# Kernel tuning notes

Hardware: AMD Instinct MI355X
Metric: run time of the kernel (lower is better)

Reference implementation:

```python
import jax, jax.numpy as jnp
import numpy as np

B, S, H = 1, 2048, 2048
E, I = 16, 1408
I_SHARED = 5632
TOP_K = 2


def setup_inputs() -> dict:
    key = jax.random.key(0)
    ks = jax.random.split(key, 8)
    scale = 0.02
    return {
        "hidden_states": jax.random.normal(ks[0], (B, S, H), dtype=jnp.float32),
        "router_w": jax.random.normal(ks[1], (H, E), dtype=jnp.float32) * scale,
        "expert_gate_up_w": jax.random.normal(ks[2], (E, H, 2 * I), dtype=jnp.float32) * scale,
        "expert_out_w": jax.random.normal(ks[3], (E, I, H), dtype=jnp.float32) * scale,
        "shared_ffw_gate_w": jax.random.normal(ks[4], (H, I_SHARED), dtype=jnp.float32) * scale,
        "shared_ffw_inter_w": jax.random.normal(ks[5], (H, I_SHARED), dtype=jnp.float32) * scale,
        "shared_ffw_out_w": jax.random.normal(ks[6], (I_SHARED, H), dtype=jnp.float32) * scale,
        "shared_gate_w": jax.random.normal(ks[7], (H, 1), dtype=jnp.float32) * scale,
        "top_k": TOP_K,
    }


def reference(hidden_states, router_w, expert_gate_up_w, expert_out_w,
              shared_ffw_gate_w, shared_ffw_inter_w, shared_ffw_out_w,
              shared_gate_w, top_k):
    b, s, h = hidden_states.shape
    e = router_w.shape[-1]
    x = hidden_states.reshape(-1, h)  # [T, H]

    # --- Router: softmax over experts, top-k, renormalize (norm_top_k_prob=True) ---
    router_logits = x @ router_w                        # [T, E]
    router_probs = jax.nn.softmax(router_logits, -1)
    top_p, top_i = jax.lax.top_k(router_probs, top_k)   # [T, K]
    top_p = top_p / jnp.sum(top_p, axis=-1, keepdims=True)
    # dense routing matrix [E, T] (matches one_hot-sum-transpose in source)
    one_hot = jax.nn.one_hot(top_i, e, dtype=top_p.dtype)  # [T, K, E]
    routing_full = jnp.sum(one_hot * top_p[..., None], axis=1).T  # [E, T]

    # --- Dense per-expert SwiGLU over ALL tokens (as in QwenMoeExperts) ---
    gate_up = jnp.einsum('th,ehm->etm', x, expert_gate_up_w)  # [E, T, 2I]
    gate, up = jnp.split(gate_up, 2, axis=-1)
    hidden = up * jax.nn.silu(gate)                           # [E, T, I]
    expert_out = jnp.einsum('eti,eih->eth', hidden, expert_out_w)  # [E, T, H]
    expert_contribution = jnp.einsum('eth,et->th', expert_out, routing_full)

    # --- Shared expert (SwiGLU MLP) with sigmoid gate ---
    sgate = jax.nn.silu(x @ shared_ffw_gate_w)
    sinter = x @ shared_ffw_inter_w
    shared_out = (sinter * sgate) @ shared_ffw_out_w          # [T, H]
    shared_out = shared_out * jax.nn.sigmoid(x @ shared_gate_w)

    out = (expert_contribution + shared_out).reshape(b, s, h)
    return out, router_logits
```

## Files before the change

kernel.cpp:

```cpp
#include <hip/hip_runtime.h>
#include <math.h>

typedef __attribute__((ext_vector_type(4))) float f32x4;
typedef __attribute__((ext_vector_type(2))) unsigned int u32x2;
typedef __attribute__((ext_vector_type(4))) unsigned int u32x4;
typedef __attribute__((ext_vector_type(8))) unsigned short u16x8;
typedef __attribute__((ext_vector_type(8))) __bf16 bf16x8;
typedef unsigned short ushort_t;

#define H_DIM 2048
#define T_TOK 2048
#define NEXP 16
#define I_DIM 1408
#define I2_DIM 2816
#define IS_DIM 5632
#define MAXROWS 6144
#define LDT 40

static __device__ __forceinline__ unsigned short f2bf(float f){
  union { float f; unsigned u; } v; v.f = f;
  unsigned r = v.u + 0x7FFFu + ((v.u >> 16) & 1u);
  return (unsigned short)(r >> 16);
}
static __device__ __forceinline__ float bf2f(unsigned short h){
  union { unsigned u; float f; } v; v.u = ((unsigned)h) << 16;
  return v.f;
}
static __device__ __forceinline__ float silu_f(float x){ return x / (1.f + __expf(-x)); }

__global__ void cast_bf16_k(const float* __restrict__ in, ushort_t* __restrict__ out){
  long i = ((long)blockIdx.x * 256 + threadIdx.x) * 8;
  f32x4 a = *(const f32x4*)&in[i];
  f32x4 b = *(const f32x4*)&in[i + 4];
  union { ushort_t s[8]; u32x4 v; } pk;
  #pragma unroll
  for (int j = 0; j < 4; j++){ pk.s[j] = f2bf(a[j]); pk.s[j+4] = f2bf(b[j]); }
  *(u32x4*)&out[i] = pk.v;
}

__global__ void transpose_cast_k(const float* __restrict__ in, ushort_t* __restrict__ out,
                                 int K, int N){
  long zo = (long)blockIdx.z * K * N;
  in += zo; out += zo;
  __shared__ float tl[32][33];
  int n0 = blockIdx.x * 32, k0 = blockIdx.y * 32;
  int tid = threadIdx.x;
  int tx = tid & 31, ty = tid >> 5;
  #pragma unroll
  for (int j = 0; j < 4; j++)
    tl[ty + j*8][tx] = in[(long)(k0 + ty + j*8) * N + n0 + tx];
  __syncthreads();
  int nl = tid >> 3, kc = (tid & 7) * 4;
  unsigned w0 = (unsigned)f2bf(tl[kc+0][nl]) | ((unsigned)f2bf(tl[kc+1][nl]) << 16);
  unsigned w1 = (unsigned)f2bf(tl[kc+2][nl]) | ((unsigned)f2bf(tl[kc+3][nl]) << 16);
  u32x2 o; o[0] = w0; o[1] = w1;
  *(u32x2*)&out[(long)(n0 + nl) * K + k0 + kc] = o;
}

__global__ void router_k(const float* __restrict__ x, const float* __restrict__ rw,
                         const float* __restrict__ sgw, float* __restrict__ logits,
                         int* __restrict__ counts, int* __restrict__ lists,
                         float* __restrict__ probs, float* __restrict__ sgmul){
  int wid = threadIdx.x >> 6, lane = threadIdx.x & 63;
  int t = blockIdx.x * 4 + wid;
  const float* xr = x + (long)t * H_DIM;
  float acc[17];
  #pragma unroll
  for (int e = 0; e < 17; e++) acc[e] = 0.f;
  for (int h0 = lane * 4; h0 < H_DIM; h0 += 256){
    f32x4 xv = *(const f32x4*)&xr[h0];
    #pragma unroll
    for (int i = 0; i < 4; i++){
      float xs = xv[i];
      const float* wrow = rw + (long)(h0 + i) * NEXP;
      #pragma unroll
      for (int e = 0; e < 16; e++) acc[e] += xs * wrow[e];
      acc[16] += xs * sgw[h0 + i];
    }
  }
  #pragma unroll
  for (int e = 0; e < 17; e++)
    for (int off = 32; off >= 1; off >>= 1)
      acc[e] += __shfl_xor(acc[e], off);
  if (lane == 0){
    float* lo = logits + (long)t * NEXP;
    #pragma unroll
    for (int e = 0; e < 16; e++) lo[e] = acc[e];
    int e0 = 0;
    #pragma unroll
    for (int e = 1; e < 16; e++) if (acc[e] > acc[e0]) e0 = e;
    int e1 = (e0 == 0) ? 1 : 0;
    #pragma unroll
    for (int e = 0; e < 16; e++) if (e != e0 && acc[e] > acc[e1]) e1 = e;
    float d = acc[e1] - acc[e0];
    float ed = __expf(d);
    float p0 = 1.f / (1.f + ed);
    float p1 = ed / (1.f + ed);
    int pos0 = atomicAdd(&counts[e0], 1);
    lists[e0 * T_TOK + pos0] = t; probs[e0 * T_TOK + pos0] = p0;
    int pos1 = atomicAdd(&counts[e1], 1);
    lists[e1 * T_TOK + pos1] = t; probs[e1 * T_TOK + pos1] = p1;
    sgmul[t] = 1.f / (1.f + __expf(-acc[16]));
  }
}

__global__ void bases_k(const int* __restrict__ counts, int* __restrict__ bases){
  if (threadIdx.x == 0){
    int r = 0;
    for (int e = 0; e < NEXP; e++){ bases[e] = r; r += (counts[e] + 127) & ~127; }
  }
}

__global__ void swiglu_expert_k(const ushort_t* __restrict__ gu, ushort_t* __restrict__ hid){
  long q = (long)blockIdx.x * 256 + threadIdx.x;
  long r = q / (I_DIM / 8); int ic = (int)(q % (I_DIM / 8)) * 8;
  const ushort_t* g = gu + r * I2_DIM + ic;
  u16x8 gv = *(const u16x8*)g;
  u16x8 uv = *(const u16x8*)(g + I_DIM);
  u16x8 ov;
  #pragma unroll
  for (int i = 0; i < 8; i++)
    ov[i] = f2bf(bf2f(uv[i]) * silu_f(bf2f(gv[i])));
  *(u16x8*)&hid[r * I_DIM + ic] = ov;
}

__global__ void swiglu_flat_k(ushort_t* __restrict__ sg, const ushort_t* __restrict__ si){
  long i = ((long)blockIdx.x * 256 + threadIdx.x) * 8;
  u16x8 g = *(const u16x8*)&sg[i];
  u16x8 s = *(const u16x8*)&si[i];
  u16x8 o;
  #pragma unroll
  for (int j = 0; j < 8; j++)
    o[j] = f2bf(bf2f(s[j]) * silu_f(bf2f(g[j])));
  *(u16x8*)&sg[i] = o;
}

template<int MODE>
__global__ void gemm_k(const ushort_t* __restrict__ A, const ushort_t* __restrict__ Bt,
                       ushort_t* __restrict__ Cb,
                       int M, int N, int K, int lda, int ldbt, int ldc,
                       const int* __restrict__ counts, const int* __restrict__ bases,
                       const int* __restrict__ lists, const float* __restrict__ probs,
                       const float* __restrict__ svec, float* __restrict__ outp,
                       long bstride){
  int z = blockIdx.z;
  int cnt = M;
  const ushort_t* Ab = A;
  const ushort_t* Bb = Bt;
  long rbase = 0;
  if constexpr (MODE == 1){ cnt = counts[z]; rbase = bases[z]; Bb += (long)z * bstride; }
  if constexpr (MODE == 2){ cnt = counts[z]; Ab += (long)bases[z] * lda; Bb += (long)z * bstride; }
  int m0 = blockIdx.y * 128;
  if (m0 >= cnt) return;
  int n0 = blockIdx.x * 128;

  __shared__ ushort_t As[128 * LDT];
  __shared__ ushort_t Bs[128 * LDT];

  int tid = threadIdx.x;
  int lane = tid & 63;
  int wr = (tid >> 7) & 1;
  int wc = (tid >> 6) & 1;

  int srow[2], skc[2];
  long aoff[2], boff[2];
  #pragma unroll
  for (int p = 0; p < 2; p++){
    int idx = p * 256 + tid;
    srow[p] = idx >> 2;
    skc[p]  = (idx & 3) * 8;
    int j = m0 + srow[p];
    if constexpr (MODE == 1){
      int jj = j < cnt ? j : cnt - 1;
      aoff[p] = (long)lists[z * T_TOK + jj] * lda + skc[p];
    } else {
      aoff[p] = (long)j * lda + skc[p];
    }
    boff[p] = (long)(n0 + srow[p]) * ldbt + skc[p];
  }

  u32x4 ar[2], br[2];
  #pragma unroll
  for (int p = 0; p < 2; p++){
    ar[p] = *(const u32x4*)(Ab + aoff[p]);
    br[p] = *(const u32x4*)(Bb + boff[p]);
  }

  f32x4 zero = {0.f, 0.f, 0.f, 0.f};
  f32x4 acc[4][4];
  #pragma unroll
  for (int i = 0; i < 4; i++)
    #pragma unroll
    for (int j = 0; j < 4; j++) acc[i][j] = zero;

  int nsteps = K / 32;
  for (int s = 0; s < nsteps; s++){
    __syncthreads();
    #pragma unroll
    for (int p = 0; p < 2; p++){
      *(u32x4*)&As[srow[p] * LDT + skc[p]] = ar[p];
      *(u32x4*)&Bs[srow[p] * LDT + skc[p]] = br[p];
    }
    __syncthreads();
    if (s + 1 < nsteps){
      int k0 = (s + 1) * 32;
      #pragma unroll
      for (int p = 0; p < 2; p++){
        ar[p] = *(const u32x4*)(Ab + aoff[p] + k0);
        br[p] = *(const u32x4*)(Bb + boff[p] + k0);
      }
    }
    bf16x8 af[4], bv[4];
    #pragma unroll
    for (int f = 0; f < 4; f++){
      af[f] = *(const bf16x8*)&As[(wr * 64 + f * 16 + (lane & 15)) * LDT + (lane >> 4) * 8];
      bv[f] = *(const bf16x8*)&Bs[(wc * 64 + f * 16 + (lane & 15)) * LDT + (lane >> 4) * 8];
    }
    #pragma unroll
    for (int fm = 0; fm < 4; fm++)
      #pragma unroll
      for (int fn = 0; fn < 4; fn++)
        acc[fm][fn] = __builtin_amdgcn_mfma_f32_16x16x32_bf16(af[fm], bv[fn], acc[fm][fn], 0, 0, 0);
  }

  int colb = n0 + wc * 64 + (lane & 15);
  int rowb = m0 + wr * 64 + (lane >> 4) * 4;
  #pragma unroll
  for (int fm = 0; fm < 4; fm++){
    #pragma unroll
    for (int fn = 0; fn < 4; fn++){
      f32x4 v = acc[fm][fn];
      int col = colb + fn * 16;
      #pragma unroll
      for (int r = 0; r < 4; r++){
        int m = rowb + fm * 16 + r;
        if constexpr (MODE == 0){
          Cb[(long)m * ldc + col] = f2bf(v[r]);
        } else if constexpr (MODE == 1){
          if (m < cnt) Cb[(rbase + m) * (long)ldc + col] = f2bf(v[r]);
        } else if constexpr (MODE == 2){
          if (m < cnt){
            int tok = lists[z * T_TOK + m];
            float p = probs[z * T_TOK + m];
            atomicAdd(outp + (long)tok * ldc + col, p * v[r]);
          }
        } else {
          outp[(long)m * ldc + col] = svec[m] * v[r];
        }
      }
    }
  }
}

extern "C" void kernel_launch(void* const* d_in, const int* in_sizes, int n_in,
                              void* d_out, int out_size, void* d_ws, size_t ws_size,
                              hipStream_t stream){
  const float* x    = (const float*)d_in[0];
  const float* rw   = (const float*)d_in[1];
  const float* wgu  = (const float*)d_in[2];
  const float* wout = (const float*)d_in[3];
  const float* wsg  = (const float*)d_in[4];
  const float* wsi  = (const float*)d_in[5];
  const float* wso  = (const float*)d_in[6];
  const float* sgw  = (const float*)d_in[7];

  float* out = (float*)d_out;
  float* logits = out + (size_t)T_TOK * H_DIM;

  char* w = (char*)d_ws;
  auto alloc = [&](size_t b){ char* p = w; w += (b + 255) & ~(size_t)255; return p; };
  ushort_t* xb     = (ushort_t*)alloc((size_t)T_TOK * H_DIM * 2);
  ushort_t* wgu_t  = (ushort_t*)alloc((size_t)NEXP * I2_DIM * H_DIM * 2);
  ushort_t* wout_t = (ushort_t*)alloc((size_t)NEXP * H_DIM * I_DIM * 2);
  ushort_t* wsg_t  = (ushort_t*)alloc((size_t)IS_DIM * H_DIM * 2);
  ushort_t* wsi_t  = (ushort_t*)alloc((size_t)IS_DIM * H_DIM * 2);
  ushort_t* wso_t  = (ushort_t*)alloc((size_t)H_DIM * IS_DIM * 2);
  ushort_t* sgr    = (ushort_t*)alloc((size_t)T_TOK * IS_DIM * 2);
  ushort_t* sir    = (ushort_t*)alloc((size_t)T_TOK * IS_DIM * 2);
  ushort_t* gu     = (ushort_t*)alloc((size_t)MAXROWS * I2_DIM * 2);
  ushort_t* hid    = (ushort_t*)alloc((size_t)MAXROWS * I_DIM * 2);
  int*   counts = (int*)alloc(64);
  int*   bases  = (int*)alloc(64);
  int*   lists  = (int*)alloc((size_t)NEXP * T_TOK * 4);
  float* probs  = (float*)alloc((size_t)NEXP * T_TOK * 4);
  float* sgmul  = (float*)alloc((size_t)T_TOK * 4);

  hipMemsetAsync(counts, 0, 64, stream);

  cast_bf16_k<<<2048, 256, 0, stream>>>(x, xb);
  transpose_cast_k<<<dim3(I2_DIM/32, H_DIM/32, NEXP), 256, 0, stream>>>(wgu, wgu_t, H_DIM, I2_DIM);
  transpose_cast_k<<<dim3(H_DIM/32, I_DIM/32, NEXP), 256, 0, stream>>>(wout, wout_t, I_DIM, H_DIM);
  transpose_cast_k<<<dim3(IS_DIM/32, H_DIM/32, 1), 256, 0, stream>>>(wsg, wsg_t, H_DIM, IS_DIM);
  transpose_cast_k<<<dim3(IS_DIM/32, H_DIM/32, 1), 256, 0, stream>>>(wsi, wsi_t, H_DIM, IS_DIM);
  transpose_cast_k<<<dim3(H_DIM/32, IS_DIM/32, 1), 256, 0, stream>>>(wso, wso_t, IS_DIM, H_DIM);

  router_k<<<512, 256, 0, stream>>>(x, rw, sgw, logits, counts, lists, probs, sgmul);
  bases_k<<<1, 64, 0, stream>>>(counts, bases);

  gemm_k<0><<<dim3(IS_DIM/128, T_TOK/128, 1), 256, 0, stream>>>(
      xb, wsg_t, sgr, T_TOK, IS_DIM, H_DIM, H_DIM, H_DIM, IS_DIM,
      nullptr, nullptr, nullptr, nullptr, nullptr, nullptr, 0);
  gemm_k<0><<<dim3(IS_DIM/128, T_TOK/128, 1), 256, 0, stream>>>(
      xb, wsi_t, sir, T_TOK, IS_DIM, H_DIM, H_DIM, H_DIM, IS_DIM,
      nullptr, nullptr, nullptr, nullptr, nullptr, nullptr, 0);
  swiglu_flat_k<<<(T_TOK * (IS_DIM/8)) / 256, 256, 0, stream>>>(sgr, sir);
  gemm_k<3><<<dim3(H_DIM/128, T_TOK/128, 1), 256, 0, stream>>>(
      sgr, wso_t, nullptr, T_TOK, H_DIM, IS_DIM, IS_DIM, IS_DIM, H_DIM,
      nullptr, nullptr, nullptr, nullptr, sgmul, out, 0);

  gemm_k<1><<<dim3(I2_DIM/128, T_TOK/128, NEXP), 256, 0, stream>>>(
      xb, wgu_t, gu, T_TOK, I2_DIM, H_DIM, H_DIM, H_DIM, I2_DIM,
      counts, bases, lists, probs, nullptr, nullptr, (long)I2_DIM * H_DIM);
  swiglu_expert_k<<<(MAXROWS * (I_DIM/8)) / 256, 256, 0, stream>>>(gu, hid);
  gemm_k<2><<<dim3(H_DIM/128, T_TOK/128, NEXP), 256, 0, stream>>>(
      hid, wout_t, nullptr, T_TOK, H_DIM, I_DIM, I_DIM, I_DIM, H_DIM,
      counts, bases, lists, probs, nullptr, out, (long)H_DIM * I_DIM);

  (void)in_sizes; (void)n_in; (void)out_size; (void)ws_size;
}
```

Baseline: 807.2 us.

## Read fp32 weights directly in GEMM, dropping separate transpose-cast pre-pass

Removes the five transpose_cast kernels that converted every weight matrix to transposed bf16 before each call. The GEMM now loads fp32 weight rows straight from the original layout, converts them to bf16 in registers, and writes them transposed into a swizzled LDS tile. The K step grows from 32 to 64, the grid is flattened with an XCD-aware block remap, and launch bounds are added. This saves a large weight read-write pass, at the cost of reading fp32 weights (twice the bytes) inside the GEMM and doing the conversion there. In MODE 1 and 2 the fp32 weights are also re-read by every M block of each expert.

```diff
diff --git a/kernel.cpp b/kernel.cpp
--- a/kernel.cpp
+++ b/kernel.cpp
@@ -1,8 +1,8 @@
 #include <hip/hip_runtime.h>
 #include <math.h>
 
+typedef __attribute__((ext_vector_type(2))) float f32x2;
 typedef __attribute__((ext_vector_type(4))) float f32x4;
-typedef __attribute__((ext_vector_type(2))) unsigned int u32x2;
 typedef __attribute__((ext_vector_type(4))) unsigned int u32x4;
 typedef __attribute__((ext_vector_type(8))) unsigned short u16x8;
 typedef __attribute__((ext_vector_type(8))) __bf16 bf16x8;
@@ -15,7 +15,6 @@
 #define I2_DIM 2816
 #define IS_DIM 5632
 #define MAXROWS 6144
-#define LDT 40
 
 static __device__ __forceinline__ unsigned short f2bf(float f){
   union { float f; unsigned u; } v; v.f = f;
@@ -27,6 +26,10 @@
   return v.f;
 }
 static __device__ __forceinline__ float silu_f(float x){ return x / (1.f + __expf(-x)); }
+
+static __device__ __forceinline__ int swz(int row, int slot){
+  return row * 64 + ((slot ^ ((row >> 1) & 7)) << 3);
+}
 
 __global__ void cast_bf16_k(const float* __restrict__ in, ushort_t* __restrict__ out){
   long i = ((long)blockIdx.x * 256 + threadIdx.x) * 8;
@@ -36,25 +39,6 @@
   #pragma unroll
   for (int j = 0; j < 4; j++){ pk.s[j] = f2bf(a[j]); pk.s[j+4] = f2bf(b[j]); }
   *(u32x4*)&out[i] = pk.v;
-}
-
-__global__ void transpose_cast_k(const float* __restrict__ in, ushort_t* __restrict__ out,
-                                 int K, int N){
-  long zo = (long)blockIdx.z * K * N;
-  in += zo; out += zo;
-  __shared__ float tl[32][33];
-  int n0 = blockIdx.x * 32, k0 = blockIdx.y * 32;
-  int tid = threadIdx.x;
-  int tx = tid & 31, ty = tid >> 5;
-  #pragma unroll
-  for (int j = 0; j < 4; j++)
-    tl[ty + j*8][tx] = in[(long)(k0 + ty + j*8) * N + n0 + tx];
-  __syncthreads();
-  int nl = tid >> 3, kc = (tid & 7) * 4;
-  unsigned w0 = (unsigned)f2bf(tl[kc+0][nl]) | ((unsigned)f2bf(tl[kc+1][nl]) << 16);
-  unsigned w1 = (unsigned)f2bf(tl[kc+2][nl]) | ((unsigned)f2bf(tl[kc+3][nl]) << 16);
-  u32x2 o; o[0] = w0; o[1] = w1;
-  *(u32x2*)&out[(long)(n0 + nl) * K + k0 + kc] = o;
 }
 
 __global__ void router_k(const float* __restrict__ x, const float* __restrict__ rw,
@@ -112,8 +96,8 @@
 }
 
 __global__ void swiglu_expert_k(const ushort_t* __restrict__ gu, ushort_t* __restrict__ hid){
-  long q = (long)blockIdx.x * 256 + threadIdx.x;
-  long r = q / (I_DIM / 8); int ic = (int)(q % (I_DIM / 8)) * 8;
+  long qd = (long)blockIdx.x * 256 + threadIdx.x;
+  long r = qd / (I_DIM / 8); int ic = (int)(qd % (I_DIM / 8)) * 8;
   const ushort_t* g = gu + r * I2_DIM + ic;
   u16x8 gv = *(const u16x8*)g;
   u16x8 uv = *(const u16x8*)(g + I_DIM);
@@ -136,54 +120,69 @@
 }
 
 template<int MODE>
-__global__ void gemm_k(const ushort_t* __restrict__ A, const ushort_t* __restrict__ Bt,
-                       ushort_t* __restrict__ Cb,
-                       int M, int N, int K, int lda, int ldbt, int ldc,
-                       const int* __restrict__ counts, const int* __restrict__ bases,
-                       const int* __restrict__ lists, const float* __restrict__ probs,
-                       const float* __restrict__ svec, float* __restrict__ outp,
-                       long bstride){
+__global__ __launch_bounds__(256, 2)
+void gemm_k(const ushort_t* __restrict__ A, const float* __restrict__ Bf,
+            ushort_t* __restrict__ Cb,
+            int K, int lda, int ldb, int ldc, int mb,
+            const int* __restrict__ counts, const int* __restrict__ bases,
+            const int* __restrict__ lists, const float* __restrict__ probs,
+            const float* __restrict__ svec, float* __restrict__ outp,
+            long bstride){
   int z = blockIdx.z;
-  int cnt = M;
+  int cnt = T_TOK;
   const ushort_t* Ab = A;
-  const ushort_t* Bb = Bt;
+  const float* Bb = Bf;
   long rbase = 0;
   if constexpr (MODE == 1){ cnt = counts[z]; rbase = bases[z]; Bb += (long)z * bstride; }
   if constexpr (MODE == 2){ cnt = counts[z]; Ab += (long)bases[z] * lda; Bb += (long)z * bstride; }
-  int m0 = blockIdx.y * 128;
+
+  int nwg = gridDim.x;
+  int wgo = blockIdx.x;
+  int q = nwg >> 3, r = nwg & 7;
+  int xcd = wgo & 7, idx = wgo >> 3;
+  int wg = (xcd < r ? xcd * (q + 1) : r * (q + 1) + (xcd - r) * q) + idx;
+  int mblk = wg % mb, nblk = wg / mb;
+  int m0 = mblk * 128;
   if (m0 >= cnt) return;
-  int n0 = blockIdx.x * 128;
-
-  __shared__ ushort_t As[128 * LDT];
-  __shared__ ushort_t Bs[128 * LDT];
+  int n0 = nblk * 128;
+
+  __shared__ ushort_t As[128 * 64];
+  __shared__ ushort_t Bs[128 * 64];
 
   int tid = threadIdx.x;
   int lane = tid & 63;
-  int wr = (tid >> 7) & 1;
-  int wc = (tid >> 6) & 1;
-
-  int srow[2], skc[2];
-  long aoff[2], boff[2];
-  #pragma unroll
-  for (int p = 0; p < 2; p++){
-    int idx = p * 256 + tid;
-    srow[p] = idx >> 2;
-    skc[p]  = (idx & 3) * 8;
-    int j = m0 + srow[p];
+  int wv = tid >> 6;
+  int wr = wv >> 1, wc = wv & 1;
+
+  const ushort_t* aptr[4];
+  int am[4], aslot[4];
+  #pragma unroll
+  for (int qq = 0; qq < 4; qq++){
+    int it = tid + qq * 256;
+    int m = it >> 3, slot = it & 7;
+    am[qq] = m; aslot[qq] = slot;
+    int row;
     if constexpr (MODE == 1){
-      int jj = j < cnt ? j : cnt - 1;
-      aoff[p] = (long)lists[z * T_TOK + jj] * lda + skc[p];
+      int j = m0 + m; if (j >= cnt) j = cnt - 1;
+      row = lists[z * T_TOK + j];
     } else {
-      aoff[p] = (long)j * lda + skc[p];
-    }
-    boff[p] = (long)(n0 + srow[p]) * ldbt + skc[p];
-  }
-
-  u32x4 ar[2], br[2];
-  #pragma unroll
-  for (int p = 0; p < 2; p++){
-    ar[p] = *(const u32x4*)(Ab + aoff[p]);
-    br[p] = *(const u32x4*)(Bb + boff[p]);
+      row = m0 + m;
+    }
+    aptr[qq] = Ab + (long)row * lda + slot * 8;
+  }
+  int p = lane;
+  int sp = wv;
+  const float* bb0 = Bb + (long)(sp * 8) * ldb + n0 + 2 * p;
+  const float* bb1 = bb0 + (long)32 * ldb;
+
+  u32x4 ar[4];
+  f32x2 br0[8], br1[8];
+  #pragma unroll
+  for (int qq = 0; qq < 4; qq++) ar[qq] = *(const u32x4*)(aptr[qq]);
+  #pragma unroll
+  for (int i = 0; i < 8; i++){
+    br0[i] = *(const f32x2*)(bb0 + (long)i * ldb);
+    br1[i] = *(const f32x2*)(bb1 + (long)i * ldb);
   }
 
   f32x4 zero = {0.f, 0.f, 0.f, 0.f};
@@ -193,34 +192,53 @@
     #pragma unroll
     for (int j = 0; j < 4; j++) acc[i][j] = zero;
 
-  int nsteps = K / 32;
+  int nsteps = K >> 6;
   for (int s = 0; s < nsteps; s++){
     __syncthreads();
     #pragma unroll
-    for (int p = 0; p < 2; p++){
-      *(u32x4*)&As[srow[p] * LDT + skc[p]] = ar[p];
-      *(u32x4*)&Bs[srow[p] * LDT + skc[p]] = br[p];
+    for (int qq = 0; qq < 4; qq++)
+      *(u32x4*)&As[swz(am[qq], aslot[qq])] = ar[qq];
+    {
+      bf16x8 c0, c1, d0, d1;
+      #pragma unroll
+      for (int i = 0; i < 8; i++){
+        c0[i] = (__bf16)br0[i][0];
+        c1[i] = (__bf16)br0[i][1];
+        d0[i] = (__bf16)br1[i][0];
+        d1[i] = (__bf16)br1[i][1];
+      }
+      *(bf16x8*)&Bs[swz(2*p,     sp)]     = c0;
+      *(bf16x8*)&Bs[swz(2*p + 1, sp)]     = c1;
+      *(bf16x8*)&Bs[swz(2*p,     sp + 4)] = d0;
+      *(bf16x8*)&Bs[swz(2*p + 1, sp + 4)] = d1;
     }
     __syncthreads();
     if (s + 1 < nsteps){
-      int k0 = (s + 1) * 32;
-      #pragma unroll
-      for (int p = 0; p < 2; p++){
-        ar[p] = *(const u32x4*)(Ab + aoff[p] + k0);
-        br[p] = *(const u32x4*)(Bb + boff[p] + k0);
+      int kt = (s + 1) * 64;
+      #pragma unroll
+      for (int qq = 0; qq < 4; qq++) ar[qq] = *(const u32x4*)(aptr[qq] + kt);
+      const float* nb0 = bb0 + (long)kt * ldb;
+      const float* nb1 = bb1 + (long)kt * ldb;
+      #pragma unroll
+      for (int i = 0; i < 8; i++){
+        br0[i] = *(const f32x2*)(nb0 + (long)i * ldb);
+        br1[i] = *(const f32x2*)(nb1 + (long)i * ldb);
       }
     }
-    bf16x8 af[4], bv[4];
-    #pragma unroll
-    for (int f = 0; f < 4; f++){
-      af[f] = *(const bf16x8*)&As[(wr * 64 + f * 16 + (lane & 15)) * LDT + (lane >> 4) * 8];
-      bv[f] = *(const bf16x8*)&Bs[(wc * 64 + f * 16 + (lane & 15)) * LDT + (lane >> 4) * 8];
-    }
-    #pragma unroll
-    for (int fm = 0; fm < 4; fm++)
-      #pragma unroll
-      for (int fn = 0; fn < 4; fn++)
-        acc[fm][fn] = __builtin_amdgcn_mfma_f32_16x16x32_bf16(af[fm], bv[fn], acc[fm][fn], 0, 0, 0);
+    #pragma unroll
+    for (int kk = 0; kk < 2; kk++){
+      bf16x8 af[4], bg[4];
+      #pragma unroll
+      for (int f = 0; f < 4; f++){
+        af[f] = *(const bf16x8*)&As[swz(wr*64 + f*16 + (lane & 15), kk*4 + (lane >> 4))];
+        bg[f] = *(const bf16x8*)&Bs[swz(wc*64 + f*16 + (lane & 15), kk*4 + (lane >> 4))];
+      }
+      #pragma unroll
+      for (int fm = 0; fm < 4; fm++)
+        #pragma unroll
+        for (int fn = 0; fn < 4; fn++)
+          acc[fm][fn] = __builtin_amdgcn_mfma_f32_16x16x32_bf16(af[fm], bg[fn], acc[fm][fn], 0, 0, 0);
+    }
   }
 
   int colb = n0 + wc * 64 + (lane & 15);
@@ -232,20 +250,20 @@
       f32x4 v = acc[fm][fn];
       int col = colb + fn * 16;
       #pragma unroll
-      for (int r = 0; r < 4; r++){
-        int m = rowb + fm * 16 + r;
+      for (int rr = 0; rr < 4; rr++){
+        int m = rowb + fm * 16 + rr;
         if constexpr (MODE == 0){
-          Cb[(long)m * ldc + col] = f2bf(v[r]);
+          Cb[(long)m * ldc + col] = f2bf(v[rr]);
         } else if constexpr (MODE == 1){
-          if (m < cnt) Cb[(rbase + m) * (long)ldc + col] = f2bf(v[r]);
+          if (m < cnt) Cb[(rbase + m) * (long)ldc + col] = f2bf(v[rr]);
         } else if constexpr (MODE == 2){
           if (m < cnt){
             int tok = lists[z * T_TOK + m];
-            float p = probs[z * T_TOK + m];
-            atomicAdd(outp + (long)tok * ldc + col, p * v[r]);
+            float pp = probs[z * T_TOK + m];
+            atomicAdd(outp + (long)tok * ldc + col, pp * v[rr]);
           }
         } else {
-          outp[(long)m * ldc + col] = svec[m] * v[r];
+          outp[(long)m * ldc + col] = svec[m] * v[rr];
         }
       }
     }
@@ -269,16 +287,11 @@
 
   char* w = (char*)d_ws;
   auto alloc = [&](size_t b){ char* p = w; w += (b + 255) & ~(size_t)255; return p; };
-  ushort_t* xb     = (ushort_t*)alloc((size_t)T_TOK * H_DIM * 2);
-  ushort_t* wgu_t  = (ushort_t*)alloc((size_t)NEXP * I2_DIM * H_DIM * 2);
-  ushort_t* wout_t = (ushort_t*)alloc((size_t)NEXP * H_DIM * I_DIM * 2);
-  ushort_t* wsg_t  = (ushort_t*)alloc((size_t)IS_DIM * H_DIM * 2);
-  ushort_t* wsi_t  = (ushort_t*)alloc((size_t)IS_DIM * H_DIM * 2);
-  ushort_t* wso_t  = (ushort_t*)alloc((size_t)H_DIM * IS_DIM * 2);
-  ushort_t* sgr    = (ushort_t*)alloc((size_t)T_TOK * IS_DIM * 2);
-  ushort_t* sir    = (ushort_t*)alloc((size_t)T_TOK * IS_DIM * 2);
-  ushort_t* gu     = (ushort_t*)alloc((size_t)MAXROWS * I2_DIM * 2);
-  ushort_t* hid    = (ushort_t*)alloc((size_t)MAXROWS * I_DIM * 2);
+  ushort_t* xb  = (ushort_t*)alloc((size_t)T_TOK * H_DIM * 2);
+  ushort_t* sgr = (ushort_t*)alloc((size_t)T_TOK * IS_DIM * 2);
+  ushort_t* sir = (ushort_t*)alloc((size_t)T_TOK * IS_DIM * 2);
+  ushort_t* gu  = (ushort_t*)alloc((size_t)MAXROWS * I2_DIM * 2);
+  ushort_t* hid = (ushort_t*)alloc((size_t)MAXROWS * I_DIM * 2);
   int*   counts = (int*)alloc(64);
   int*   bases  = (int*)alloc(64);
   int*   lists  = (int*)alloc((size_t)NEXP * T_TOK * 4);
@@ -288,33 +301,27 @@
   hipMemsetAsync(counts, 0, 64, stream);
 
   cast_bf16_k<<<2048, 256, 0, stream>>>(x, xb);
-  transpose_cast_k<<<dim3(I2_DIM/32, H_DIM/32, NEXP), 256, 0, stream>>>(wgu, wgu_t, H_DIM, I2_DIM);
-  transpose_cast_k<<<dim3(H_DIM/32, I_DIM/32, NEXP), 256, 0, stream>>>(wout, wout_t, I_DIM, H_DIM);
-  transpose_cast_k<<<dim3(IS_DIM/32, H_DIM/32, 1), 256, 0, stream>>>(wsg, wsg_t, H_DIM, IS_DIM);
-  transpose_cast_k<<<dim3(IS_DIM/32, H_DIM/32, 1), 256, 0, stream>>>(wsi, wsi_t, H_DIM, IS_DIM);
-  transpose_cast_k<<<dim3(H_DIM/32, IS_DIM/32, 1), 256, 0, stream>>>(wso, wso_t, IS_DIM, H_DIM);
-
   router_k<<<512, 256, 0, stream>>>(x, rw, sgw, logits, counts, lists, probs, sgmul);
   bases_k<<<1, 64, 0, stream>>>(counts, bases);
 
-  gemm_k<0><<<dim3(IS_DIM/128, T_TOK/128, 1), 256, 0, stream>>>(
-      xb, wsg_t, sgr, T_TOK, IS_DIM, H_DIM, H_DIM, H_DIM, IS_DIM,
+  gemm_k<0><<<dim3((IS_DIM/128) * (T_TOK/128), 1, 1), 256, 0, stream>>>(
+      xb, wsg, sgr, H_DIM, H_DIM, IS_DIM, IS_DIM, T_TOK/128,
       nullptr, nullptr, nullptr, nullptr, nullptr, nullptr, 0);
-  gemm_k<0><<<dim3(IS_DIM/128, T_TOK/128, 1), 256, 0, stream>>>(
-      xb, wsi_t, sir, T_TOK, IS_DIM, H_DIM, H_DIM, H_DIM, IS_DIM,
+  gemm_k<0><<<dim3((IS_DIM/128) * (T_TOK/128), 1, 1), 256, 0, stream>>>(
+      xb, wsi, sir, H_DIM, H_DIM, IS_DIM, IS_DIM, T_TOK/128,
       nullptr, nullptr, nullptr, nullptr, nullptr, nullptr, 0);
   swiglu_flat_k<<<(T_TOK * (IS_DIM/8)) / 256, 256, 0, stream>>>(sgr, sir);
-  gemm_k<3><<<dim3(H_DIM/128, T_TOK/128, 1), 256, 0, stream>>>(
-      sgr, wso_t, nullptr, T_TOK, H_DIM, IS_DIM, IS_DIM, IS_DIM, H_DIM,
+  gemm_k<3><<<dim3((H_DIM/128) * (T_TOK/128), 1, 1), 256, 0, stream>>>(
+      sgr, wso, nullptr, IS_DIM, IS_DIM, H_DIM, H_DIM, T_TOK/128,
       nullptr, nullptr, nullptr, nullptr, sgmul, out, 0);
 
-  gemm_k<1><<<dim3(I2_DIM/128, T_TOK/128, NEXP), 256, 0, stream>>>(
-      xb, wgu_t, gu, T_TOK, I2_DIM, H_DIM, H_DIM, H_DIM, I2_DIM,
-      counts, bases, lists, probs, nullptr, nullptr, (long)I2_DIM * H_DIM);
+  gemm_k<1><<<dim3((I2_DIM/128) * (T_TOK/128), 1, NEXP), 256, 0, stream>>>(
+      xb, wgu, gu, H_DIM, H_DIM, I2_DIM, I2_DIM, T_TOK/128,
+      counts, bases, lists, probs, nullptr, nullptr, (long)H_DIM * I2_DIM);
   swiglu_expert_k<<<(MAXROWS * (I_DIM/8)) / 256, 256, 0, stream>>>(gu, hid);
-  gemm_k<2><<<dim3(H_DIM/128, T_TOK/128, NEXP), 256, 0, stream>>>(
-      hid, wout_t, nullptr, T_TOK, H_DIM, I_DIM, I_DIM, I_DIM, H_DIM,
-      counts, bases, lists, probs, nullptr, out, (long)H_DIM * I_DIM);
+  gemm_k<2><<<dim3((H_DIM/128) * (T_TOK/128), 1, NEXP), 256, 0, stream>>>(
+      hid, wout, nullptr, I_DIM, I_DIM, H_DIM, H_DIM, T_TOK/128,
+      counts, bases, lists, probs, nullptr, out, (long)I_DIM * H_DIM);
 
   (void)in_sizes; (void)n_in; (void)out_size; (void)ws_size;
 }
```

New measurement: 826.2 us. 2.4% more time.

## Use direct global-to-LDS loads, XCD-aware tile remap, split-K and batched shared GEMMs

Applied to the files above, without the earlier changes.

Replaces register-staged tile loads with global_load_lds direct-to-LDS copies using an unpadded 32-wide LDS layout, and drops the register prefetch. Remaps flat block indices so that neighbouring tiles land on the same XCD for L2 reuse. Fuses the two shared gate/inter GEMMs into one launch via grid z, and splits K in two for the shared output GEMM, which now accumulates with atomics into a pre-zeroed output. This removes the register round trip but loses load/compute overlap, and the unpadded LDS may cause bank conflicts. The split-K path also adds atomic traffic and a memset.

```diff
diff --git a/kernel.cpp b/kernel.cpp
--- a/kernel.cpp
+++ b/kernel.cpp
@@ -15,7 +15,6 @@
 #define I2_DIM 2816
 #define IS_DIM 5632
 #define MAXROWS 6144
-#define LDT 40
 
 static __device__ __forceinline__ unsigned short f2bf(float f){
   union { float f; unsigned u; } v; v.f = f;
@@ -27,6 +26,12 @@
   return v.f;
 }
 static __device__ __forceinline__ float silu_f(float x){ return x / (1.f + __expf(-x)); }
+
+static __device__ __forceinline__ void gld16(const ushort_t* g, ushort_t* l){
+  __builtin_amdgcn_global_load_lds(
+      (const __attribute__((address_space(1))) unsigned int*)g,
+      (__attribute__((address_space(3))) unsigned int*)l, 16, 0, 0);
+}
 
 __global__ void cast_bf16_k(const float* __restrict__ in, ushort_t* __restrict__ out){
   long i = ((long)blockIdx.x * 256 + threadIdx.x) * 8;
@@ -112,8 +117,8 @@
 }
 
 __global__ void swiglu_expert_k(const ushort_t* __restrict__ gu, ushort_t* __restrict__ hid){
-  long q = (long)blockIdx.x * 256 + threadIdx.x;
-  long r = q / (I_DIM / 8); int ic = (int)(q % (I_DIM / 8)) * 8;
+  long qd = (long)blockIdx.x * 256 + threadIdx.x;
+  long r = qd / (I_DIM / 8); int ic = (int)(qd % (I_DIM / 8)) * 8;
   const ushort_t* g = gu + r * I2_DIM + ic;
   u16x8 gv = *(const u16x8*)g;
   u16x8 uv = *(const u16x8*)(g + I_DIM);
@@ -136,54 +141,64 @@
 }
 
 template<int MODE>
-__global__ void gemm_k(const ushort_t* __restrict__ A, const ushort_t* __restrict__ Bt,
-                       ushort_t* __restrict__ Cb,
-                       int M, int N, int K, int lda, int ldbt, int ldc,
-                       const int* __restrict__ counts, const int* __restrict__ bases,
-                       const int* __restrict__ lists, const float* __restrict__ probs,
-                       const float* __restrict__ svec, float* __restrict__ outp,
-                       long bstride){
+__global__ __launch_bounds__(256)
+void gemm_k(const ushort_t* __restrict__ A, const ushort_t* __restrict__ Bt,
+            const ushort_t* __restrict__ Bt2, ushort_t* __restrict__ Cb,
+            int K, int lda, int ldbt, int ldc, int mb,
+            const int* __restrict__ counts, const int* __restrict__ bases,
+            const int* __restrict__ lists, const float* __restrict__ probs,
+            const float* __restrict__ svec, float* __restrict__ outp,
+            long bstride){
   int z = blockIdx.z;
-  int cnt = M;
+  int cnt = T_TOK;
   const ushort_t* Ab = A;
   const ushort_t* Bb = Bt;
   long rbase = 0;
+  if constexpr (MODE == 0){ if (z){ Bb = Bt2; Cb += (long)T_TOK * ldc; } }
   if constexpr (MODE == 1){ cnt = counts[z]; rbase = bases[z]; Bb += (long)z * bstride; }
   if constexpr (MODE == 2){ cnt = counts[z]; Ab += (long)bases[z] * lda; Bb += (long)z * bstride; }
-  int m0 = blockIdx.y * 128;
+
+  int kb = K / gridDim.y;
+  int kbase = blockIdx.y * kb;
+  Ab += kbase;
+  Bb += kbase;
+
+  int nwg = gridDim.x;
+  int wgo = blockIdx.x;
+  int q = nwg >> 3, r = nwg & 7;
+  int xcd = wgo & 7, idx = wgo >> 3;
+  int wg = (xcd < r ? xcd * (q + 1) : r * (q + 1) + (xcd - r) * q) + idx;
+  int mblk = wg % mb, nblk = wg / mb;
+  int m0 = mblk * 128;
   if (m0 >= cnt) return;
-  int n0 = blockIdx.x * 128;
-
-  __shared__ ushort_t As[128 * LDT];
-  __shared__ ushort_t Bs[128 * LDT];
+  int n0 = nblk * 128;
+
+  __shared__ ushort_t As[128 * 32];
+  __shared__ ushort_t Bs[128 * 32];
 
   int tid = threadIdx.x;
   int lane = tid & 63;
-  int wr = (tid >> 7) & 1;
-  int wc = (tid >> 6) & 1;
-
-  int srow[2], skc[2];
+  int wv = tid >> 6;
+  int wr = wv >> 1, wc = wv & 1;
+
+  int crow = lane >> 2;
+  int kcol = (lane & 3) * 8;
   long aoff[2], boff[2];
-  #pragma unroll
-  for (int p = 0; p < 2; p++){
-    int idx = p * 256 + tid;
-    srow[p] = idx >> 2;
-    skc[p]  = (idx & 3) * 8;
-    int j = m0 + srow[p];
+  ushort_t* lA[2]; ushort_t* lB[2];
+  #pragma unroll
+  for (int c = 0; c < 2; c++){
+    int mr = wv * 32 + c * 16 + crow;
+    int grow;
     if constexpr (MODE == 1){
-      int jj = j < cnt ? j : cnt - 1;
-      aoff[p] = (long)lists[z * T_TOK + jj] * lda + skc[p];
+      int j = m0 + mr; if (j >= cnt) j = cnt - 1;
+      grow = lists[z * T_TOK + j];
     } else {
-      aoff[p] = (long)j * lda + skc[p];
+      grow = m0 + mr;
     }
-    boff[p] = (long)(n0 + srow[p]) * ldbt + skc[p];
-  }
-
-  u32x4 ar[2], br[2];
-  #pragma unroll
-  for (int p = 0; p < 2; p++){
-    ar[p] = *(const u32x4*)(Ab + aoff[p]);
-    br[p] = *(const u32x4*)(Bb + boff[p]);
+    aoff[c] = (long)grow * lda + kcol;
+    boff[c] = (long)(n0 + mr) * ldbt + kcol;
+    lA[c] = As + (wv * 32 + c * 16) * 32;
+    lB[c] = Bs + (wv * 32 + c * 16) * 32;
   }
 
   f32x4 zero = {0.f, 0.f, 0.f, 0.f};
@@ -193,34 +208,26 @@
     #pragma unroll
     for (int j = 0; j < 4; j++) acc[i][j] = zero;
 
-  int nsteps = K / 32;
+  int nsteps = kb >> 5;
   for (int s = 0; s < nsteps; s++){
     __syncthreads();
-    #pragma unroll
-    for (int p = 0; p < 2; p++){
-      *(u32x4*)&As[srow[p] * LDT + skc[p]] = ar[p];
-      *(u32x4*)&Bs[srow[p] * LDT + skc[p]] = br[p];
-    }
+    int kof = s * 32;
+    gld16(Ab + aoff[0] + kof, lA[0]);
+    gld16(Ab + aoff[1] + kof, lA[1]);
+    gld16(Bb + boff[0] + kof, lB[0]);
+    gld16(Bb + boff[1] + kof, lB[1]);
     __syncthreads();
-    if (s + 1 < nsteps){
-      int k0 = (s + 1) * 32;
-      #pragma unroll
-      for (int p = 0; p < 2; p++){
-        ar[p] = *(const u32x4*)(Ab + aoff[p] + k0);
-        br[p] = *(const u32x4*)(Bb + boff[p] + k0);
-      }
-    }
-    bf16x8 af[4], bv[4];
+    bf16x8 af[4], bg[4];
     #pragma unroll
     for (int f = 0; f < 4; f++){
-      af[f] = *(const bf16x8*)&As[(wr * 64 + f * 16 + (lane & 15)) * LDT + (lane >> 4) * 8];
-      bv[f] = *(const bf16x8*)&Bs[(wc * 64 + f * 16 + (lane & 15)) * LDT + (lane >> 4) * 8];
+      af[f] = *(const bf16x8*)&As[(wr*64 + f*16 + (lane & 15)) * 32 + (lane >> 4) * 8];
+      bg[f] = *(const bf16x8*)&Bs[(wc*64 + f*16 + (lane & 15)) * 32 + (lane >> 4) * 8];
     }
     #pragma unroll
     for (int fm = 0; fm < 4; fm++)
       #pragma unroll
       for (int fn = 0; fn < 4; fn++)
-        acc[fm][fn] = __builtin_amdgcn_mfma_f32_16x16x32_bf16(af[fm], bv[fn], acc[fm][fn], 0, 0, 0);
+        acc[fm][fn] = __builtin_amdgcn_mfma_f32_16x16x32_bf16(af[fm], bg[fn], acc[fm][fn], 0, 0, 0);
   }
 
   int colb = n0 + wc * 64 + (lane & 15);
@@ -232,20 +239,20 @@
       f32x4 v = acc[fm][fn];
       int col = colb + fn * 16;
       #pragma unroll
-      for (int r = 0; r < 4; r++){
-        int m = rowb + fm * 16 + r;
+      for (int rr = 0; rr < 4; rr++){
+        int m = rowb + fm * 16 + rr;
         if constexpr (MODE == 0){
-          Cb[(long)m * ldc + col] = f2bf(v[r]);
+          Cb[(long)m * ldc + col] = f2bf(v[rr]);
         } else if constexpr (MODE == 1){
-          if (m < cnt) Cb[(rbase + m) * (long)ldc + col] = f2bf(v[r]);
+          if (m < cnt) Cb[(rbase + m) * (long)ldc + col] = f2bf(v[rr]);
         } else if constexpr (MODE == 2){
           if (m < cnt){
             int tok = lists[z * T_TOK + m];
-            float p = probs[z * T_TOK + m];
-            atomicAdd(outp + (long)tok * ldc + col, p * v[r]);
+            float pp = probs[z * T_TOK + m];
+            atomicAdd(outp + (long)tok * ldc + col, pp * v[rr]);
           }
         } else {
-          outp[(long)m * ldc + col] = svec[m] * v[r];
+          atomicAdd(outp + (long)m * ldc + col, svec[m] * v[rr]);
         }
       }
     }
@@ -275,8 +282,8 @@
   ushort_t* wsg_t  = (ushort_t*)alloc((size_t)IS_DIM * H_DIM * 2);
   ushort_t* wsi_t  = (ushort_t*)alloc((size_t)IS_DIM * H_DIM * 2);
   ushort_t* wso_t  = (ushort_t*)alloc((size_t)H_DIM * IS_DIM * 2);
-  ushort_t* sgr    = (ushort_t*)alloc((size_t)T_TOK * IS_DIM * 2);
-  ushort_t* sir    = (ushort_t*)alloc((size_t)T_TOK * IS_DIM * 2);
+  ushort_t* sgr    = (ushort_t*)alloc((size_t)2 * T_TOK * IS_DIM * 2);
+  ushort_t* sir    = sgr + (size_t)T_TOK * IS_DIM;
   ushort_t* gu     = (ushort_t*)alloc((size_t)MAXROWS * I2_DIM * 2);
   ushort_t* hid    = (ushort_t*)alloc((size_t)MAXROWS * I_DIM * 2);
   int*   counts = (int*)alloc(64);
@@ -286,6 +293,7 @@
   float* sgmul  = (float*)alloc((size_t)T_TOK * 4);
 
   hipMemsetAsync(counts, 0, 64, stream);
+  hipMemsetAsync(out, 0, (size_t)T_TOK * H_DIM * sizeof(float), stream);
 
   cast_bf16_k<<<2048, 256, 0, stream>>>(x, xb);
   transpose_cast_k<<<dim3(I2_DIM/32, H_DIM/32, NEXP), 256, 0, stream>>>(wgu, wgu_t, H_DIM, I2_DIM);
@@ -297,23 +305,20 @@
   router_k<<<512, 256, 0, stream>>>(x, rw, sgw, logits, counts, lists, probs, sgmul);
   bases_k<<<1, 64, 0, stream>>>(counts, bases);
 
-  gemm_k<0><<<dim3(IS_DIM/128, T_TOK/128, 1), 256, 0, stream>>>(
-      xb, wsg_t, sgr, T_TOK, IS_DIM, H_DIM, H_DIM, H_DIM, IS_DIM,
-      nullptr, nullptr, nullptr, nullptr, nullptr, nullptr, 0);
-  gemm_k<0><<<dim3(IS_DIM/128, T_TOK/128, 1), 256, 0, stream>>>(
-      xb, wsi_t, sir, T_TOK, IS_DIM, H_DIM, H_DIM, H_DIM, IS_DIM,
+  gemm_k<0><<<dim3((IS_DIM/128) * (T_TOK/128), 1, 2), 256, 0, stream>>>(
+      xb, wsg_t, wsi_t, sgr, H_DIM, H_DIM, H_DIM, IS_DIM, T_TOK/128,
       nullptr, nullptr, nullptr, nullptr, nullptr, nullptr, 0);
   swiglu_flat_k<<<(T_TOK * (IS_DIM/8)) / 256, 256, 0, stream>>>(sgr, sir);
-  gemm_k<3><<<dim3(H_DIM/128, T_TOK/128, 1), 256, 0, stream>>>(
-      sgr, wso_t, nullptr, T_TOK, H_DIM, IS_DIM, IS_DIM, IS_DIM, H_DIM,
+  gemm_k<3><<<dim3((H_DIM/128) * (T_TOK/128), 2, 1), 256, 0, stream>>>(
+      sgr, wso_t, nullptr, nullptr, IS_DIM, IS_DIM, IS_DIM, H_DIM, T_TOK/128,
       nullptr, nullptr, nullptr, nullptr, sgmul, out, 0);
 
-  gemm_k<1><<<dim3(I2_DIM/128, T_TOK/128, NEXP), 256, 0, stream>>>(
-      xb, wgu_t, gu, T_TOK, I2_DIM, H_DIM, H_DIM, H_DIM, I2_DIM,
+  gemm_k<1><<<dim3((I2_DIM/128) * (T_TOK/128), 1, NEXP), 256, 0, stream>>>(
+      xb, wgu_t, nullptr, gu, H_DIM, H_DIM, H_DIM, I2_DIM, T_TOK/128,
       counts, bases, lists, probs, nullptr, nullptr, (long)I2_DIM * H_DIM);
   swiglu_expert_k<<<(MAXROWS * (I_DIM/8)) / 256, 256, 0, stream>>>(gu, hid);
-  gemm_k<2><<<dim3(H_DIM/128, T_TOK/128, NEXP), 256, 0, stream>>>(
-      hid, wout_t, nullptr, T_TOK, H_DIM, I_DIM, I_DIM, I_DIM, H_DIM,
+  gemm_k<2><<<dim3((H_DIM/128) * (T_TOK/128), 1, NEXP), 256, 0, stream>>>(
+      hid, wout_t, nullptr, nullptr, I_DIM, I_DIM, I_DIM, H_DIM, T_TOK/128,
       counts, bases, lists, probs, nullptr, out, (long)H_DIM * I_DIM);
 
   (void)in_sizes; (void)n_in; (void)out_size; (void)ws_size;
```

Measured after the change: 861.6 us. +6.7%, slower.
